# Performance work log

Hardware: AMD Instinct MI355X
Metric: run time of the kernel (lower is better)

## Reference

```python
import jax, jax.numpy as jnp
import numpy as np

B, S, H = 4, 2048, 1536
NH, HD = 12, 128          # num_heads, head_dim
K = 4                     # base_kernel
INNER = 4 * H             # GLU inner dim
EPS = 1e-6
CONV_DILS = (1, 2, 4, 8, 16, 32)
HEAD_DILS = [(1, 2, 4), (1, 1, 1), (4, 8, 16), (8, 16, 32), (32, 64, 128),
             (64, 128, 256), (256, 512, 1024), (1, 100, 200), (1, 500, 1000),
             (1, 1024, 2048), (3, 9, 27), (5, 25, 125)]


def setup_inputs() -> dict:
    key = jax.random.key(0)
    ks = jax.random.split(key, 20)
    sd = 0.02
    inp = {
        'x': jax.random.normal(ks[0], (B, S, H), dtype=jnp.float32),
        'norm_w': jnp.ones((3, H), dtype=jnp.float32),
        # DilatedConvStack: 6 depthwise convs (C=H, K=4) + proj Linear(H,H)
        'conv_ws': jax.random.normal(ks[1], (6, H, 1, K), dtype=jnp.float32) * sd,
        'conv_bs': jax.random.normal(ks[2], (6, H), dtype=jnp.float32) * sd,
        'conv_proj_w': jax.random.normal(ks[3], (H, H), dtype=jnp.float32) * sd,
        'conv_proj_b': jax.random.normal(ks[4], (H,), dtype=jnp.float32) * sd,
        # MultiHeadDilatedState
        'gate_w': jax.random.normal(ks[5], (2 * H, H), dtype=jnp.float32) * sd,
        'router_w': jax.random.normal(ks[6], (NH, H), dtype=jnp.float32) * sd,
        'router_b': jax.random.normal(ks[7], (NH,), dtype=jnp.float32) * sd,
        'head_ws': jax.random.normal(ks[8], (NH, 3, HD, 1, K), dtype=jnp.float32) * sd,
        'head_bs': jax.random.normal(ks[9], (NH, 3, HD), dtype=jnp.float32) * sd,
        'mix_gate_w': jax.random.normal(ks[10], (H, H), dtype=jnp.float32) * sd,
        'mix_gate_b': jnp.full((H,), 2.0, dtype=jnp.float32),
        'mixing_w': jax.random.normal(ks[11], (H, H), dtype=jnp.float32) * sd,
        'mixing_b': jax.random.normal(ks[12], (H,), dtype=jnp.float32) * sd,
        # GLU FFN
        'ffn_in_w': jax.random.normal(ks[13], (2 * INNER, H), dtype=jnp.float32) * sd,
        'ffn_out_w': jax.random.normal(ks[14], (H, INNER), dtype=jnp.float32) * sd,
        # path gates (Linear(H,1) x 3)
        'pg_w': jax.random.normal(ks[15], (3, H), dtype=jnp.float32) * sd,
        'pg_b': jnp.full((3,), 2.0, dtype=jnp.float32),
    }
    return inp


def rmsnorm(x, w):
    norm = jax.lax.rsqrt(jnp.mean(x * x, axis=-1, keepdims=True) + EPS)
    return x * norm * w


def dconv(h, w, b, d):
    # h: [B, C, S], w: [C, 1, K] depthwise, causal left-pad (K-1)*d
    C = h.shape[1]
    pad = (K - 1) * d
    y = jax.lax.conv_general_dilated(
        h, w, window_strides=(1,), padding=[(pad, 0)], rhs_dilation=(d,),
        dimension_numbers=('NCH', 'OIH', 'NCH'), feature_group_count=C)
    return y + b[None, :, None]


def reference(x, norm_w, conv_ws, conv_bs, conv_proj_w, conv_proj_b,
              gate_w, router_w, router_b, head_ws, head_bs,
              mix_gate_w, mix_gate_b, mixing_w, mixing_b,
              ffn_in_w, ffn_out_w, pg_w, pg_b):
    n1 = rmsnorm(x, norm_w[0])
    n2 = rmsnorm(x, norm_w[1])
    n3 = rmsnorm(x, norm_w[2])
    gc = jax.nn.sigmoid(jnp.einsum('bsh,h->bs', n1, pg_w[0]) + pg_b[0])[..., None]
    gs = jax.nn.sigmoid(jnp.einsum('bsh,h->bs', n2, pg_w[1]) + pg_b[1])[..., None]
    gf = jax.nn.sigmoid(jnp.einsum('bsh,h->bs', n3, pg_w[2]) + pg_b[2])[..., None]

    # --- DilatedConvStack path ---
    h = jnp.swapaxes(n1, 1, 2)  # [B, H, S]
    for i, d in enumerate(CONV_DILS):
        h = h + jax.nn.gelu(dconv(h, conv_ws[i], conv_bs[i], d), approximate=False)
    conv_out = jnp.swapaxes(h, 1, 2) @ conv_proj_w.T + conv_proj_b
    x = x + gc * conv_out

    # --- MultiHeadDilatedState path ---
    head_weights = jax.nn.sigmoid(n2 @ router_w.T + router_b)  # [B, S, NH]
    g = n2 @ gate_w.T                                          # [B, S, 2H]
    content, gate = jnp.split(g, 2, axis=-1)
    x_gated = content * jax.nn.sigmoid(gate)
    x_heads = x_gated.reshape(B, S, NH, HD)
    outs = []
    for i in range(NH):
        hh = jnp.swapaxes(x_heads[:, :, i, :], 1, 2)  # [B, HD, S]
        for j, d in enumerate(HEAD_DILS[i]):
            hh = hh + dconv(hh, head_ws[i, j], head_bs[i, j], d)
        hh = jnp.swapaxes(hh, 1, 2)                   # [B, S, HD]
        outs.append(hh * head_weights[:, :, i:i + 1])
    out = jnp.concatenate(outs, axis=-1)              # [B, S, H]
    out = out * jax.nn.sigmoid(out @ mix_gate_w.T + mix_gate_b)
    state_out = out @ mixing_w.T + mixing_b
    x = x + gs * state_out

    # --- GLU FFN path ---
    hff = n3 @ ffn_in_w.T
    c, gt = jnp.split(hff, 2, axis=-1)
    ffn_out = (c * jax.nn.sigmoid(gt)) @ ffn_out_w.T
    x = x + gf * ffn_out
    return x
```

## Files before the change

### kernel.cpp

```cpp
#include <hip/hip_runtime.h>
#include <stdint.h>

#define H 1536
#define SQ 2048
#define BB 4
#define MT 8192
#define NHD 12
#define INNER 6144
#define EPSF 1e-6f

typedef unsigned short u16;
typedef __bf16 b16x8 __attribute__((ext_vector_type(8)));
typedef float f32x4 __attribute__((ext_vector_type(4)));

__device__ __forceinline__ u16 f2b(float f) {
  uint32_t u = __float_as_uint(f);
  u = u + 0x7fffu + ((u >> 16) & 1u);
  return (u16)(u >> 16);
}
__device__ __forceinline__ float b2f(u16 u) { return __uint_as_float(((uint32_t)u) << 16); }
__device__ __forceinline__ float sigm(float x) { return 1.0f / (1.0f + __expf(-x)); }
__device__ __forceinline__ float gelu_exact(float x) {
  float z = fabsf(x) * 0.70710678118654752f;
  float t = 1.0f / (1.0f + 0.3275911f * z);
  float p = t * (0.254829592f + t * (-0.284496736f + t * (1.421413741f +
            t * (-1.453152027f + t * 1.061405429f))));
  float erfa = 1.0f - p * __expf(-z * z);
  float erfv = (x >= 0.f) ? erfa : -erfa;
  return 0.5f * x * (1.0f + erfv);
}
__device__ __forceinline__ void load_lds16(const void* g, void* l) {
  __builtin_amdgcn_global_load_lds(
      (__attribute__((address_space(1))) void*)(g),
      (__attribute__((address_space(3))) void*)(l), 16, 0, 0);
}

__global__ __launch_bounds__(256) void k_rmsnorm(const float* __restrict__ x, u16* __restrict__ xb) {
  int m = blockIdx.x, t = threadIdx.x;
  const float* row = x + (size_t)m * H;
  float v[6]; float ss = 0.f;
#pragma unroll
  for (int j = 0; j < 6; ++j) { v[j] = row[t + j * 256]; ss += v[j] * v[j]; }
#pragma unroll
  for (int o = 32; o > 0; o >>= 1) ss += __shfl_xor(ss, o);
  __shared__ float red[4];
  if ((t & 63) == 0) red[t >> 6] = ss;
  __syncthreads();
  float r = rsqrtf((red[0] + red[1] + red[2] + red[3]) / (float)H + EPSF);
#pragma unroll
  for (int j = 0; j < 6; ++j) xb[(size_t)m * H + t + j * 256] = f2b(v[j] * r);
}

__global__ __launch_bounds__(256) void k_gates(const u16* __restrict__ xb, const float* __restrict__ norm_w,
    const float* __restrict__ pg_w, const float* __restrict__ pg_b,
    const float* __restrict__ router_w, const float* __restrict__ router_b,
    float* __restrict__ gates, float* __restrict__ hw) {
  int m = blockIdx.x, t = threadIdx.x;
  const u16* row = xb + (size_t)m * H;
  float acc[15];
#pragma unroll
  for (int i = 0; i < 15; ++i) acc[i] = 0.f;
  for (int j = 0; j < 6; ++j) {
    int c = t + j * 256;
    float xv = b2f(row[c]);
    float n0 = norm_w[c], n1 = norm_w[H + c], n2 = norm_w[2 * H + c];
    acc[0] += xv * n0 * pg_w[c];
    acc[1] += xv * n1 * pg_w[H + c];
    acc[2] += xv * n2 * pg_w[2 * H + c];
    float xn = xv * n1;
#pragma unroll
    for (int i = 0; i < 12; ++i) acc[3 + i] += xn * router_w[(size_t)i * H + c];
  }
  __shared__ float red[15][4];
#pragma unroll
  for (int i = 0; i < 15; ++i) {
    float s = acc[i];
#pragma unroll
    for (int o = 32; o > 0; o >>= 1) s += __shfl_xor(s, o);
    if ((t & 63) == 0) red[i][t >> 6] = s;
  }
  __syncthreads();
  if (t < 15) {
    float s = red[t][0] + red[t][1] + red[t][2] + red[t][3];
    if (t < 3) gates[t * MT + m] = sigm(s + pg_b[t]);
    else hw[(size_t)m * NHD + (t - 3)] = sigm(s + router_b[t - 3]);
  }
}

__global__ __launch_bounds__(256) void k_wcvt(const float* __restrict__ w, u16* __restrict__ wb,
                                              const float* __restrict__ cs, int K) {
  int c = blockIdx.x * 256 + threadIdx.x;
  size_t r = blockIdx.y;
  float v = w[r * K + c];
  if (cs) v *= cs[c];
  wb[r * K + c] = f2b(v);
}
__global__ __launch_bounds__(256) void k_wcvt2(const float* __restrict__ w, u16* __restrict__ wb,
                                               const float* __restrict__ cs, int K, int HALF) {
  int c = blockIdx.x * 256 + threadIdx.x;
  int rr = blockIdx.y;
  int src = (rr & 1) ? (HALF + (rr >> 1)) : (rr >> 1);
  wb[(size_t)rr * K + c] = f2b(w[(size_t)src * K + c] * cs[c]);
}

__global__ __launch_bounds__(256) void k_conv(const u16* __restrict__ in, u16* __restrict__ out,
    const float* __restrict__ w, const float* __restrict__ bias, int d, const float* __restrict__ insc) {
  int c = blockIdx.x * 256 + threadIdx.x;
  int s0 = blockIdx.y * 8, b = blockIdx.z;
  float sc = insc ? insc[c] : 1.f;
  const u16* base = in + (size_t)b * SQ * H + c;
  u16* obase = out + (size_t)b * SQ * H + c;
  float4 wv = *(const float4*)(w + (size_t)c * 4);
  float bv = bias[c];
#pragma unroll
  for (int k = 0; k < 8; ++k) {
    int s = s0 + k;
    float center = b2f(base[(size_t)s * H]) * sc;
    float acc = bv + wv.w * center;
    if (s - d     >= 0) acc += wv.z * b2f(base[(size_t)(s - d) * H]) * sc;
    if (s - 2 * d >= 0) acc += wv.y * b2f(base[(size_t)(s - 2 * d) * H]) * sc;
    if (s - 3 * d >= 0) acc += wv.x * b2f(base[(size_t)(s - 3 * d) * H]) * sc;
    obase[(size_t)s * H] = f2b(center + gelu_exact(acc));
  }
}

__constant__ int HDILS[36] = {1,2,4, 1,1,1, 4,8,16, 8,16,32, 32,64,128, 64,128,256,
                              256,512,1024, 1,100,200, 1,500,1000, 1,1024,2048, 3,9,27, 5,25,125};

__global__ __launch_bounds__(256) void k_hconv(const u16* __restrict__ in, u16* __restrict__ out,
    const float* __restrict__ hws, const float* __restrict__ hbs, int j, const float* __restrict__ hwp) {
  int c = blockIdx.x * 256 + threadIdx.x;
  int s0 = blockIdx.y * 8, b = blockIdx.z;
  int head = c >> 7, cc = c & 127;
  int d = HDILS[head * 3 + j];
  size_t wi = (size_t)(head * 3 + j) * 128 + cc;
  float4 wv = *(const float4*)(hws + wi * 4);
  float bv = hbs[wi];
  const u16* base = in + (size_t)b * SQ * H + c;
  u16* obase = out + (size_t)b * SQ * H + c;
#pragma unroll
  for (int k = 0; k < 8; ++k) {
    int s = s0 + k;
    float center = b2f(base[(size_t)s * H]);
    float acc = bv + wv.w * center;
    if (s - d     >= 0) acc += wv.z * b2f(base[(size_t)(s - d) * H]);
    if (s - 2 * d >= 0) acc += wv.y * b2f(base[(size_t)(s - 2 * d) * H]);
    if (s - 3 * d >= 0) acc += wv.x * b2f(base[(size_t)(s - 3 * d) * H]);
    float v = center + acc;
    if (hwp) v *= hwp[((size_t)b * SQ + s) * NHD + head];
    obase[(size_t)s * H] = f2b(v);
  }
}

#define MMQ(AF, BF, MO, NO)                                                      \
  _Pragma("unroll") for (int m_ = 0; m_ < 4; ++m_)                               \
  _Pragma("unroll") for (int n_ = 0; n_ < 2; ++n_)                               \
  _Pragma("unroll") for (int ks_ = 0; ks_ < 2; ++ks_)                            \
    acc[(MO) + m_][(NO) + n_] = __builtin_amdgcn_mfma_f32_16x16x32_bf16(         \
        AF[m_][ks_], BF[n_][ks_], acc[(MO) + m_][(NO) + n_], 0, 0, 0);

#define TILE(BUF, SKO, DOSTAGE, VMSTMT)                                          \
  {                                                                              \
    b16x8 alo[4][2], ahi[4][2], blo[2][2], bhi[2][2];                            \
    _Pragma("unroll") for (int m = 0; m < 4; ++m) {                              \
      alo[m][0] = *(const b16x8*)(Ard0 + (BUF) * 16384 + m * 1024);              \
      alo[m][1] = *(const b16x8*)(Ard1 + (BUF) * 16384 + m * 1024);              \
    }                                                                            \
    _Pragma("unroll") for (int n = 0; n < 2; ++n) {                              \
      blo[n][0] = *(const b16x8*)(Brd0 + (BUF) * 16384 + n * 1024);              \
      blo[n][1] = *(const b16x8*)(Brd1 + (BUF) * 16384 + n * 1024);              \
    }                                                                            \
    asm volatile("s_waitcnt lgkmcnt(8)" ::: "memory");                           \
    __builtin_amdgcn_sched_barrier(0);                                           \
    __builtin_amdgcn_s_barrier();                                                \
    asm volatile("s_waitcnt lgkmcnt(0)" ::: "memory");                           \
    __builtin_amdgcn_sched_barrier(0);                                           \
    __builtin_amdgcn_s_setprio(1);                                               \
    MMQ(alo, blo, 0, 0);                                                         \
    __builtin_amdgcn_s_setprio(0);                                               \
    __builtin_amdgcn_sched_barrier(0);                                           \
    __builtin_amdgcn_s_barrier();                                                \
    _Pragma("unroll") for (int n = 0; n < 2; ++n) {                              \
      bhi[n][0] = *(const b16x8*)(Brd0 + (BUF) * 16384 + 2048 + n * 1024);       \
      bhi[n][1] = *(const b16x8*)(Brd1 + (BUF) * 16384 + 2048 + n * 1024);       \
    }                                                                            \
    __builtin_amdgcn_sched_barrier(0);                                           \
    __builtin_amdgcn_s_barrier();                                                \
    asm volatile("s_waitcnt lgkmcnt(0)" ::: "memory");                           \
    __builtin_amdgcn_sched_barrier(0);                                           \
    __builtin_amdgcn_s_setprio(1);                                               \
    MMQ(alo, bhi, 0, 2);                                                         \
    __builtin_amdgcn_s_setprio(0);                                               \
    __builtin_amdgcn_sched_barrier(0);                                           \
    __builtin_amdgcn_s_barrier();                                                \
    _Pragma("unroll") for (int m = 0; m < 4; ++m) {                              \
      ahi[m][0] = *(const b16x8*)(Ard0 + (BUF) * 16384 + 4096 + m * 1024);       \
      ahi[m][1] = *(const b16x8*)(Ard1 + (BUF) * 16384 + 4096 + m * 1024);       \
    }                                                                            \
    if (DOSTAGE) {                                                               \
      load_lds16(Bg + (boff0 + (SKO)), dB0 + (BUF) * 16384);                     \
      load_lds16(Bg + (boff1 + (SKO)), dB1 + (BUF) * 16384);                     \
      load_lds16(Bg + (boff2 + (SKO)), dB2 + (BUF) * 16384);                     \
      load_lds16(Bg + (boff3 + (SKO)), dB3 + (BUF) * 16384);                     \
    }                                                                            \
    __builtin_amdgcn_sched_barrier(0);                                           \
    __builtin_amdgcn_s_barrier();                                                \
    asm volatile("s_waitcnt lgkmcnt(0)" ::: "memory");                           \
    __builtin_amdgcn_sched_barrier(0);                                           \
    __builtin_amdgcn_s_setprio(1);                                               \
    MMQ(ahi, bhi, 4, 2);                                                         \
    __builtin_amdgcn_s_setprio(0);                                               \
    __builtin_amdgcn_sched_barrier(0);                                           \
    __builtin_amdgcn_s_barrier();                                                \
    if (DOSTAGE) {                                                               \
      load_lds16(Ag + (aoff0 + (SKO)), dA0 + (BUF) * 16384);                     \
      load_lds16(Ag + (aoff1 + (SKO)), dA1 + (BUF) * 16384);                     \
      load_lds16(Ag + (aoff2 + (SKO)), dA2 + (BUF) * 16384);                     \
      load_lds16(Ag + (aoff3 + (SKO)), dA3 + (BUF) * 16384);                     \
    }                                                                            \
    __builtin_amdgcn_sched_barrier(0);                                           \
    __builtin_amdgcn_s_barrier();                                                \
    __builtin_amdgcn_s_setprio(1);                                               \
    MMQ(ahi, blo, 4, 0);                                                         \
    __builtin_amdgcn_s_setprio(0);                                               \
    VMSTMT;                                                                      \
    __builtin_amdgcn_sched_barrier(0);                                           \
    __builtin_amdgcn_s_barrier();                                                \
  }

template<int MODE>
__global__ __launch_bounds__(512, 2) void k_gemm(const u16* __restrict__ A, int lda,
    const u16* __restrict__ B, int ldb, void* __restrict__ Cout, int M, int N, int K,
    const float* __restrict__ bias, const float* __restrict__ gate, const u16* __restrict__ aux,
    const float* __restrict__ xres) {
  __shared__ u16 lds[65536];
  int tid = threadIdx.x;
  int w = tid >> 6, lane = tid & 63;
  int l15 = lane & 15, l4 = lane >> 4;
  int wr = w >> 2, wc = w & 3;

  int gx = gridDim.x, gy = gridDim.y;
  int nwg = gx * gy;
  int bid = blockIdx.y * gx + blockIdx.x;
  int bm, bn;
  if (((nwg & 7) == 0) && ((gy & 7) == 0)) {
    int xcd = bid & 7, l = bid >> 3;
    int rpx = gy >> 3;
    bm = xcd * rpx + (l % rpx);
    bn = l / rpx;
  } else { bn = bid % gx; bm = bid / gx; }

  const u16* Ag = A + (size_t)bm * 256 * lda;
  const u16* Bg = B + (size_t)bn * 256 * ldb;
  int nt = K >> 6;

  f32x4 acc[8][4];
#pragma unroll
  for (int m = 0; m < 8; ++m)
#pragma unroll
    for (int n = 0; n < 4; ++n) acc[m][n] = f32x4{0.f, 0.f, 0.f, 0.f};

  int m7 = l15 & 7;
  int slot0 = l4 ^ m7, slot1 = slot0 ^ 4;
  const u16* Ard0 = lds + wr * 8192 + l15 * 64 + slot0 * 8;
  const u16* Ard1 = lds + wr * 8192 + l15 * 64 + slot1 * 8;
  const u16* Brd0 = lds + 32768 + (wc >> 1) * 8192 + ((wc & 1) * 64 + l15) * 64 + slot0 * 8;
  const u16* Brd1 = lds + 32768 + (wc >> 1) * 8192 + ((wc & 1) * 64 + l15) * 64 + slot1 * 8;

  int r0 = tid >> 3;
  int kg = ((lane & 7) ^ (lane >> 3)) * 8;
  int aoff0 = (0 * 128 + 0 * 64 + r0) * lda + kg;
  int aoff1 = (0 * 128 + 1 * 64 + r0) * lda + kg;
  int aoff2 = (1 * 128 + 0 * 64 + r0) * lda + kg;
  int aoff3 = (1 * 128 + 1 * 64 + r0) * lda + kg;
  int boff0 = (0 * 128 + 0 * 64 + r0) * ldb + kg;
  int boff1 = (0 * 128 + 1 * 64 + r0) * ldb + kg;
  int boff2 = (1 * 128 + 0 * 64 + r0) * ldb + kg;
  int boff3 = (1 * 128 + 1 * 64 + r0) * ldb + kg;
  int w512 = w * 512;
  u16* dA0 = lds + 0 * 4096 + w512;
  u16* dA1 = lds + 1 * 4096 + w512;
  u16* dA2 = lds + 2 * 4096 + w512;
  u16* dA3 = lds + 3 * 4096 + w512;
  u16* dB0 = lds + 32768 + 0 * 4096 + w512;
  u16* dB1 = lds + 32768 + 1 * 4096 + w512;
  u16* dB2 = lds + 32768 + 2 * 4096 + w512;
  u16* dB3 = lds + 32768 + 3 * 4096 + w512;

  load_lds16(Bg + boff0, dB0); load_lds16(Bg + boff1, dB1);
  load_lds16(Bg + boff2, dB2); load_lds16(Bg + boff3, dB3);
  load_lds16(Ag + aoff0, dA0); load_lds16(Ag + aoff1, dA1);
  load_lds16(Ag + aoff2, dA2); load_lds16(Ag + aoff3, dA3);
  load_lds16(Bg + boff0 + 64, dB0 + 16384); load_lds16(Bg + boff1 + 64, dB1 + 16384);
  load_lds16(Bg + boff2 + 64, dB2 + 16384); load_lds16(Bg + boff3 + 64, dB3 + 16384);
  load_lds16(Ag + aoff0 + 64, dA0 + 16384); load_lds16(Ag + aoff1 + 64, dA1 + 16384);
  load_lds16(Ag + aoff2 + 64, dA2 + 16384); load_lds16(Ag + aoff3 + 64, dA3 + 16384);
  asm volatile("s_waitcnt vmcnt(8)" ::: "memory");
  __builtin_amdgcn_s_barrier();
  __builtin_amdgcn_sched_barrier(0);

  int koff = 0;
  int main_iters = (nt >> 1) - 1;
  for (int it = 0; it < main_iters; ++it) {
    TILE(0, koff + 128, true, asm volatile("s_waitcnt vmcnt(8)" ::: "memory"));
    TILE(1, koff + 192, true, asm volatile("s_waitcnt vmcnt(8)" ::: "memory"));
    koff += 128;
  }
  TILE(0, 0, false, asm volatile("s_waitcnt vmcnt(0)" ::: "memory"));
  TILE(1, 0, false, (void)0);

  int rowbase = bm * 256 + wr * 128;
  int colbase = bn * 256 + wc * 64;
#pragma unroll
  for (int n = 0; n < 4; ++n) {
    int col = colbase + n * 16 + l15;
    float bv = (MODE == 2) ? 0.f : (bias ? bias[col] : 0.f);
#pragma unroll
    for (int m = 0; m < 8; ++m) {
#pragma unroll
      for (int j = 0; j < 4; ++j) {
        int r = rowbase + m * 16 + l4 * 4 + j;
        float val = acc[m][n][j];
        if (MODE == 0) {
          size_t idx = (size_t)r * N + col;
          ((float*)Cout)[idx] = xres[idx] + (val + bv) * gate[r];
        } else if (MODE == 1) {
          ((float*)Cout)[(size_t)r * N + col] += (val + bv) * (gate ? gate[r] : 1.f);
        } else if (MODE == 2) {
          float other = __shfl_xor(val, 1);
          if ((lane & 1) == 0)
            ((u16*)Cout)[(size_t)r * (N >> 1) + (col >> 1)] = f2b(val * sigm(other));
        } else {
          float a = b2f(aux[(size_t)r * N + col]);
          ((u16*)Cout)[(size_t)r * N + col] = f2b(a * sigm(val + bv));
        }
      }
    }
  }
}

extern "C" void kernel_launch(void* const* d_in, const int* in_sizes, int n_in,
                              void* d_out, int out_size, void* d_ws, size_t ws_size,
                              hipStream_t stream) {
  const float* x        = (const float*)d_in[0];
  const float* norm_w   = (const float*)d_in[1];
  const float* conv_ws  = (const float*)d_in[2];
  const float* conv_bs  = (const float*)d_in[3];
  const float* conv_pw  = (const float*)d_in[4];
  const float* conv_pb  = (const float*)d_in[5];
  const float* gate_w   = (const float*)d_in[6];
  const float* router_w = (const float*)d_in[7];
  const float* router_b = (const float*)d_in[8];
  const float* head_ws  = (const float*)d_in[9];
  const float* head_bs  = (const float*)d_in[10];
  const float* mixg_w   = (const float*)d_in[11];
  const float* mixg_b   = (const float*)d_in[12];
  const float* mix_w    = (const float*)d_in[13];
  const float* mix_b    = (const float*)d_in[14];
  const float* ffn_iw   = (const float*)d_in[15];
  const float* ffn_ow   = (const float*)d_in[16];
  const float* pg_w     = (const float*)d_in[17];
  const float* pg_b     = (const float*)d_in[18];
  float* out = (float*)d_out;

  char* ws = (char*)d_ws;
  size_t o = 0;
  auto alloc = [&](size_t n) { char* p = ws + o; o += n; return p; };
  u16*  XB  = (u16*)alloc(25165824);
  u16*  A16 = (u16*)alloc(25165824);
  u16*  B16 = (u16*)alloc(25165824);
  u16*  WG2 = (u16*)alloc(9437184);
  u16*  WP  = (u16*)alloc(4718592);
  u16*  WMG = (u16*)alloc(4718592);
  u16*  WMX = (u16*)alloc(4718592);
  u16*  WFI = (u16*)alloc(37748736);
  u16*  WFO = (u16*)alloc(18874368);
  float* gates = (float*)alloc(98304);
  float* hw    = (float*)alloc(393216);
  u16*  VB = A16;

  k_rmsnorm<<<MT, 256, 0, stream>>>(x, XB);
  k_gates<<<MT, 256, 0, stream>>>(XB, norm_w, pg_w, pg_b, router_w, router_b, gates, hw);

  k_wcvt2<<<dim3(6, 3072),  256, 0, stream>>>(gate_w, WG2, norm_w + H, H, H);
  k_wcvt <<<dim3(6, 1536),  256, 0, stream>>>(conv_pw, WP, nullptr, H);
  k_wcvt <<<dim3(6, 1536),  256, 0, stream>>>(mixg_w, WMG, nullptr, H);
  k_wcvt <<<dim3(6, 1536),  256, 0, stream>>>(mix_w, WMX, nullptr, H);
  k_wcvt2<<<dim3(6, 12288), 256, 0, stream>>>(ffn_iw, WFI, norm_w + 2 * H, H, INNER);
  k_wcvt <<<dim3(24, 1536), 256, 0, stream>>>(ffn_ow, WFO, nullptr, INNER);

  dim3 cg(6, SQ / 8, BB);
  k_conv<<<cg, 256, 0, stream>>>(XB,  A16, conv_ws + 0 * H * 4, conv_bs + 0 * H, 1,  norm_w);
  k_conv<<<cg, 256, 0, stream>>>(A16, B16, conv_ws + 1 * H * 4, conv_bs + 1 * H, 2,  nullptr);
  k_conv<<<cg, 256, 0, stream>>>(B16, A16, conv_ws + 2 * H * 4, conv_bs + 2 * H, 4,  nullptr);
  k_conv<<<cg, 256, 0, stream>>>(A16, B16, conv_ws + 3 * H * 4, conv_bs + 3 * H, 8,  nullptr);
  k_conv<<<cg, 256, 0, stream>>>(B16, A16, conv_ws + 4 * H * 4, conv_bs + 4 * H, 16, nullptr);
  k_conv<<<cg, 256, 0, stream>>>(A16, B16, conv_ws + 5 * H * 4, conv_bs + 5 * H, 32, nullptr);
  k_gemm<0><<<dim3(6, 32), 512, 0, stream>>>(B16, H, WP, H, out, MT, H, H, conv_pb, gates, nullptr, x);

  k_gemm<2><<<dim3(12, 32), 512, 0, stream>>>(XB, H, WG2, H, A16, MT, 2 * H, H, nullptr, nullptr, nullptr, nullptr);
  k_hconv<<<cg, 256, 0, stream>>>(A16, B16, head_ws, head_bs, 0, nullptr);
  k_hconv<<<cg, 256, 0, stream>>>(B16, A16, head_ws, head_bs, 1, nullptr);
  k_hconv<<<cg, 256, 0, stream>>>(A16, B16, head_ws, head_bs, 2, hw);
  k_gemm<3><<<dim3(6, 32), 512, 0, stream>>>(B16, H, WMG, H, A16, MT, H, H, mixg_b, nullptr, B16, nullptr);
  k_gemm<1><<<dim3(6, 32), 512, 0, stream>>>(A16, H, WMX, H, out, MT, H, H, mix_b, gates + MT, nullptr, nullptr);

  for (int ch = 0; ch < 2; ++ch) {
    k_gemm<2><<<dim3(24, 32), 512, 0, stream>>>(XB, H, WFI + (size_t)ch * 6144 * H, H,
                                                VB, MT, 6144, H, nullptr, nullptr, nullptr, nullptr);
    k_gemm<1><<<dim3(6, 32), 512, 0, stream>>>(VB, 3072, WFO + ch * 3072, INNER,
                                               out, MT, H, 3072, nullptr, gates + 2 * MT, nullptr, nullptr);
  }
}
```

Baseline: 1.317 ms.

## Fuse pairs of dilated conv layers and batch gate rows per block

Pairs of consecutive dilated depthwise convolutions (the six conv-stack layers and the first two head-conv layers) now run in one kernel each. Every output recomputes the four first-layer taps it needs, which removes an intermediate bf16 round trip through global memory and some launches. The cost is about four times the first-layer loads and GELU evaluations per output, now done by one thread per sequence position. The gates kernel handles 16 rows per block and precomputes the norm-weight products once per block. The three HxH weight conversions are merged into a single launch.

```diff
diff --git a/kernel.cpp b/kernel.cpp
--- a/kernel.cpp
+++ b/kernel.cpp
@@ -51,39 +51,50 @@
   for (int j = 0; j < 6; ++j) xb[(size_t)m * H + t + j * 256] = f2b(v[j] * r);
 }
 
-__global__ __launch_bounds__(256) void k_gates(const u16* __restrict__ xb, const float* __restrict__ norm_w,
+__global__ __launch_bounds__(256) void k_gates16(const u16* __restrict__ xb, const float* __restrict__ norm_w,
     const float* __restrict__ pg_w, const float* __restrict__ pg_b,
     const float* __restrict__ router_w, const float* __restrict__ router_b,
     float* __restrict__ gates, float* __restrict__ hw) {
-  int m = blockIdx.x, t = threadIdx.x;
-  const u16* row = xb + (size_t)m * H;
-  float acc[15];
-#pragma unroll
-  for (int i = 0; i < 15; ++i) acc[i] = 0.f;
+  int t = threadIdx.x;
+  int m0 = blockIdx.x * 16;
+  float pm[6][15];
+#pragma unroll
   for (int j = 0; j < 6; ++j) {
     int c = t + j * 256;
-    float xv = b2f(row[c]);
     float n0 = norm_w[c], n1 = norm_w[H + c], n2 = norm_w[2 * H + c];
-    acc[0] += xv * n0 * pg_w[c];
-    acc[1] += xv * n1 * pg_w[H + c];
-    acc[2] += xv * n2 * pg_w[2 * H + c];
-    float xn = xv * n1;
-#pragma unroll
-    for (int i = 0; i < 12; ++i) acc[3 + i] += xn * router_w[(size_t)i * H + c];
+    pm[j][0] = n0 * pg_w[c];
+    pm[j][1] = n1 * pg_w[H + c];
+    pm[j][2] = n2 * pg_w[2 * H + c];
+#pragma unroll
+    for (int i = 0; i < 12; ++i) pm[j][3 + i] = n1 * router_w[(size_t)i * H + c];
   }
   __shared__ float red[15][4];
-#pragma unroll
-  for (int i = 0; i < 15; ++i) {
-    float s = acc[i];
-#pragma unroll
-    for (int o = 32; o > 0; o >>= 1) s += __shfl_xor(s, o);
-    if ((t & 63) == 0) red[i][t >> 6] = s;
-  }
-  __syncthreads();
-  if (t < 15) {
-    float s = red[t][0] + red[t][1] + red[t][2] + red[t][3];
-    if (t < 3) gates[t * MT + m] = sigm(s + pg_b[t]);
-    else hw[(size_t)m * NHD + (t - 3)] = sigm(s + router_b[t - 3]);
+  for (int tk = 0; tk < 16; ++tk) {
+    int m = m0 + tk;
+    const u16* row = xb + (size_t)m * H;
+    float acc[15];
+#pragma unroll
+    for (int i = 0; i < 15; ++i) acc[i] = 0.f;
+#pragma unroll
+    for (int j = 0; j < 6; ++j) {
+      float xv = b2f(row[t + j * 256]);
+#pragma unroll
+      for (int i = 0; i < 15; ++i) acc[i] += xv * pm[j][i];
+    }
+#pragma unroll
+    for (int i = 0; i < 15; ++i) {
+      float s = acc[i];
+#pragma unroll
+      for (int o = 32; o > 0; o >>= 1) s += __shfl_xor(s, o);
+      if ((t & 63) == 0) red[i][t >> 6] = s;
+    }
+    __syncthreads();
+    if (t < 15) {
+      float s = red[t][0] + red[t][1] + red[t][2] + red[t][3];
+      if (t < 3) gates[t * MT + m] = sigm(s + pg_b[t]);
+      else hw[(size_t)m * NHD + (t - 3)] = sigm(s + router_b[t - 3]);
+    }
+    __syncthreads();
   }
 }
 
@@ -102,30 +113,74 @@
   int src = (rr & 1) ? (HALF + (rr >> 1)) : (rr >> 1);
   wb[(size_t)rr * K + c] = f2b(w[(size_t)src * K + c] * cs[c]);
 }
-
-__global__ __launch_bounds__(256) void k_conv(const u16* __restrict__ in, u16* __restrict__ out,
-    const float* __restrict__ w, const float* __restrict__ bias, int d, const float* __restrict__ insc) {
-  int c = blockIdx.x * 256 + threadIdx.x;
-  int s0 = blockIdx.y * 8, b = blockIdx.z;
+__global__ __launch_bounds__(256) void k_wcvt3(const float* __restrict__ w0, const float* __restrict__ w1,
+                                               const float* __restrict__ w2, u16* __restrict__ wb) {
+  int c = blockIdx.x * 256 + threadIdx.x;
+  int r = blockIdx.y;
+  const float* src = (r < 1536) ? w0 : (r < 3072 ? w1 : w2);
+  int rr = (r < 1536) ? r : (r < 3072 ? r - 1536 : r - 3072);
+  wb[(size_t)r * H + c] = f2b(src[(size_t)rr * H + c]);
+}
+
+__global__ __launch_bounds__(256) void k_conv2(const u16* __restrict__ in, u16* __restrict__ out,
+    const float* __restrict__ w0p, const float* __restrict__ b0p,
+    const float* __restrict__ w1p, const float* __restrict__ b1p,
+    int d0, int d1, const float* __restrict__ insc) {
+  int c = blockIdx.x * 256 + threadIdx.x;
+  int s = blockIdx.y, b = blockIdx.z;
   float sc = insc ? insc[c] : 1.f;
   const u16* base = in + (size_t)b * SQ * H + c;
-  u16* obase = out + (size_t)b * SQ * H + c;
-  float4 wv = *(const float4*)(w + (size_t)c * 4);
-  float bv = bias[c];
-#pragma unroll
-  for (int k = 0; k < 8; ++k) {
-    int s = s0 + k;
-    float center = b2f(base[(size_t)s * H]) * sc;
-    float acc = bv + wv.w * center;
-    if (s - d     >= 0) acc += wv.z * b2f(base[(size_t)(s - d) * H]) * sc;
-    if (s - 2 * d >= 0) acc += wv.y * b2f(base[(size_t)(s - 2 * d) * H]) * sc;
-    if (s - 3 * d >= 0) acc += wv.x * b2f(base[(size_t)(s - 3 * d) * H]) * sc;
-    obase[(size_t)s * H] = f2b(center + gelu_exact(acc));
-  }
+  float4 wv0 = *(const float4*)(w0p + (size_t)c * 4);
+  float4 wv1 = *(const float4*)(w1p + (size_t)c * 4);
+  float b0 = b0p[c], b1 = b1p[c];
+  float h1v[4];
+#pragma unroll
+  for (int k = 0; k < 4; ++k) {
+    int r = s - k * d1;
+    if (r >= 0) {
+      float center = b2f(base[(size_t)r * H]) * sc;
+      float a = b0 + wv0.w * center;
+      if (r - d0     >= 0) a += wv0.z * b2f(base[(size_t)(r - d0) * H]) * sc;
+      if (r - 2 * d0 >= 0) a += wv0.y * b2f(base[(size_t)(r - 2 * d0) * H]) * sc;
+      if (r - 3 * d0 >= 0) a += wv0.x * b2f(base[(size_t)(r - 3 * d0) * H]) * sc;
+      h1v[k] = center + gelu_exact(a);
+    } else h1v[k] = 0.f;
+  }
+  float a1 = b1 + wv1.w * h1v[0] + wv1.z * h1v[1] + wv1.y * h1v[2] + wv1.x * h1v[3];
+  out[((size_t)b * SQ + s) * H + c] = f2b(h1v[0] + gelu_exact(a1));
 }
 
 __constant__ int HDILS[36] = {1,2,4, 1,1,1, 4,8,16, 8,16,32, 32,64,128, 64,128,256,
                               256,512,1024, 1,100,200, 1,500,1000, 1,1024,2048, 3,9,27, 5,25,125};
+
+__global__ __launch_bounds__(256) void k_hconv2(const u16* __restrict__ in, u16* __restrict__ out,
+    const float* __restrict__ hws, const float* __restrict__ hbs) {
+  int c = blockIdx.x * 256 + threadIdx.x;
+  int s = blockIdx.y, b = blockIdx.z;
+  int head = c >> 7, cc = c & 127;
+  int d0 = HDILS[head * 3 + 0], d1 = HDILS[head * 3 + 1];
+  size_t wi0 = (size_t)(head * 3 + 0) * 128 + cc;
+  size_t wi1 = (size_t)(head * 3 + 1) * 128 + cc;
+  float4 wv0 = *(const float4*)(hws + wi0 * 4);
+  float4 wv1 = *(const float4*)(hws + wi1 * 4);
+  float b0 = hbs[wi0], b1 = hbs[wi1];
+  const u16* base = in + (size_t)b * SQ * H + c;
+  float h1v[4];
+#pragma unroll
+  for (int k = 0; k < 4; ++k) {
+    int r = s - k * d1;
+    if (r >= 0) {
+      float center = b2f(base[(size_t)r * H]);
+      float a = b0 + wv0.w * center;
+      if (r - d0     >= 0) a += wv0.z * b2f(base[(size_t)(r - d0) * H]);
+      if (r - 2 * d0 >= 0) a += wv0.y * b2f(base[(size_t)(r - 2 * d0) * H]);
+      if (r - 3 * d0 >= 0) a += wv0.x * b2f(base[(size_t)(r - 3 * d0) * H]);
+      h1v[k] = center + a;
+    } else h1v[k] = 0.f;
+  }
+  float a1 = b1 + wv1.w * h1v[0] + wv1.z * h1v[1] + wv1.y * h1v[2] + wv1.x * h1v[3];
+  out[((size_t)b * SQ + s) * H + c] = f2b(h1v[0] + a1);
+}
 
 __global__ __launch_bounds__(256) void k_hconv(const u16* __restrict__ in, u16* __restrict__ out,
     const float* __restrict__ hws, const float* __restrict__ hbs, int j, const float* __restrict__ hwp) {
@@ -380,28 +435,25 @@
   u16*  VB = A16;
 
   k_rmsnorm<<<MT, 256, 0, stream>>>(x, XB);
-  k_gates<<<MT, 256, 0, stream>>>(XB, norm_w, pg_w, pg_b, router_w, router_b, gates, hw);
+  k_gates16<<<MT / 16, 256, 0, stream>>>(XB, norm_w, pg_w, pg_b, router_w, router_b, gates, hw);
 
   k_wcvt2<<<dim3(6, 3072),  256, 0, stream>>>(gate_w, WG2, norm_w + H, H, H);
-  k_wcvt <<<dim3(6, 1536),  256, 0, stream>>>(conv_pw, WP, nullptr, H);
-  k_wcvt <<<dim3(6, 1536),  256, 0, stream>>>(mixg_w, WMG, nullptr, H);
-  k_wcvt <<<dim3(6, 1536),  256, 0, stream>>>(mix_w, WMX, nullptr, H);
+  k_wcvt3<<<dim3(6, 4608),  256, 0, stream>>>(conv_pw, mixg_w, mix_w, WP);
   k_wcvt2<<<dim3(6, 12288), 256, 0, stream>>>(ffn_iw, WFI, norm_w + 2 * H, H, INNER);
   k_wcvt <<<dim3(24, 1536), 256, 0, stream>>>(ffn_ow, WFO, nullptr, INNER);
 
-  dim3 cg(6, SQ / 8, BB);
-  k_conv<<<cg, 256, 0, stream>>>(XB,  A16, conv_ws + 0 * H * 4, conv_bs + 0 * H, 1,  norm_w);
-  k_conv<<<cg, 256, 0, stream>>>(A16, B16, conv_ws + 1 * H * 4, conv_bs + 1 * H, 2,  nullptr);
-  k_conv<<<cg, 256, 0, stream>>>(B16, A16, conv_ws + 2 * H * 4, conv_bs + 2 * H, 4,  nullptr);
-  k_conv<<<cg, 256, 0, stream>>>(A16, B16, conv_ws + 3 * H * 4, conv_bs + 3 * H, 8,  nullptr);
-  k_conv<<<cg, 256, 0, stream>>>(B16, A16, conv_ws + 4 * H * 4, conv_bs + 4 * H, 16, nullptr);
-  k_conv<<<cg, 256, 0, stream>>>(A16, B16, conv_ws + 5 * H * 4, conv_bs + 5 * H, 32, nullptr);
-  k_gemm<0><<<dim3(6, 32), 512, 0, stream>>>(B16, H, WP, H, out, MT, H, H, conv_pb, gates, nullptr, x);
-
-  k_gemm<2><<<dim3(12, 32), 512, 0, stream>>>(XB, H, WG2, H, A16, MT, 2 * H, H, nullptr, nullptr, nullptr, nullptr);
-  k_hconv<<<cg, 256, 0, stream>>>(A16, B16, head_ws, head_bs, 0, nullptr);
-  k_hconv<<<cg, 256, 0, stream>>>(B16, A16, head_ws, head_bs, 1, nullptr);
-  k_hconv<<<cg, 256, 0, stream>>>(A16, B16, head_ws, head_bs, 2, hw);
+  dim3 cg1(6, SQ, BB);
+  k_conv2<<<cg1, 256, 0, stream>>>(XB,  A16, conv_ws + 0 * H * 4, conv_bs + 0 * H,
+                                   conv_ws + 1 * H * 4, conv_bs + 1 * H, 1, 2, norm_w);
+  k_conv2<<<cg1, 256, 0, stream>>>(A16, B16, conv_ws + 2 * H * 4, conv_bs + 2 * H,
+                                   conv_ws + 3 * H * 4, conv_bs + 3 * H, 4, 8, nullptr);
+  k_conv2<<<cg1, 256, 0, stream>>>(B16, A16, conv_ws + 4 * H * 4, conv_bs + 4 * H,
+                                   conv_ws + 5 * H * 4, conv_bs + 5 * H, 16, 32, nullptr);
+  k_gemm<0><<<dim3(6, 32), 512, 0, stream>>>(A16, H, WP, H, out, MT, H, H, conv_pb, gates, nullptr, x);
+
+  k_gemm<2><<<dim3(12, 32), 512, 0, stream>>>(XB, H, WG2, H, B16, MT, 2 * H, H, nullptr, nullptr, nullptr, nullptr);
+  k_hconv2<<<cg1, 256, 0, stream>>>(B16, A16, head_ws, head_bs);
+  k_hconv<<<dim3(6, SQ / 8, BB), 256, 0, stream>>>(A16, B16, head_ws, head_bs, 2, hw);
   k_gemm<3><<<dim3(6, 32), 512, 0, stream>>>(B16, H, WMG, H, A16, MT, H, H, mixg_b, nullptr, B16, nullptr);
   k_gemm<1><<<dim3(6, 32), 512, 0, stream>>>(A16, H, WMX, H, out, MT, H, H, mix_b, gates + MT, nullptr, nullptr);
 
```

Result: slower. 1.464 ms (+11.2%).

## Batch gate rows per block, merge weight casts, unchunk FFN when workspace allows

Applied to the files above, without the earlier changes.

The gates kernel now handles 16 rows per block and precomputes the norm-weighted projection coefficients once per block rather than once per row. The three square weight conversions are merged into a single launch. When the workspace can hold the full GLU intermediate, the FFN runs as one up-projection GEMM and one down-projection GEMM instead of two chunks of each, which cuts launches and read-modify-write passes over the output. The cost is an extra 96MB workspace buffer and a K=6144 down-projection GEMM whose single accumulation pass may behave differently.

```diff
diff --git a/kernel.cpp b/kernel.cpp
--- a/kernel.cpp
+++ b/kernel.cpp
@@ -51,39 +51,50 @@
   for (int j = 0; j < 6; ++j) xb[(size_t)m * H + t + j * 256] = f2b(v[j] * r);
 }
 
-__global__ __launch_bounds__(256) void k_gates(const u16* __restrict__ xb, const float* __restrict__ norm_w,
+__global__ __launch_bounds__(256) void k_gates16(const u16* __restrict__ xb, const float* __restrict__ norm_w,
     const float* __restrict__ pg_w, const float* __restrict__ pg_b,
     const float* __restrict__ router_w, const float* __restrict__ router_b,
     float* __restrict__ gates, float* __restrict__ hw) {
-  int m = blockIdx.x, t = threadIdx.x;
-  const u16* row = xb + (size_t)m * H;
-  float acc[15];
-#pragma unroll
-  for (int i = 0; i < 15; ++i) acc[i] = 0.f;
+  int t = threadIdx.x;
+  int m0 = blockIdx.x * 16;
+  float pm[6][15];
+#pragma unroll
   for (int j = 0; j < 6; ++j) {
     int c = t + j * 256;
-    float xv = b2f(row[c]);
     float n0 = norm_w[c], n1 = norm_w[H + c], n2 = norm_w[2 * H + c];
-    acc[0] += xv * n0 * pg_w[c];
-    acc[1] += xv * n1 * pg_w[H + c];
-    acc[2] += xv * n2 * pg_w[2 * H + c];
-    float xn = xv * n1;
-#pragma unroll
-    for (int i = 0; i < 12; ++i) acc[3 + i] += xn * router_w[(size_t)i * H + c];
+    pm[j][0] = n0 * pg_w[c];
+    pm[j][1] = n1 * pg_w[H + c];
+    pm[j][2] = n2 * pg_w[2 * H + c];
+#pragma unroll
+    for (int i = 0; i < 12; ++i) pm[j][3 + i] = n1 * router_w[(size_t)i * H + c];
   }
   __shared__ float red[15][4];
-#pragma unroll
-  for (int i = 0; i < 15; ++i) {
-    float s = acc[i];
-#pragma unroll
-    for (int o = 32; o > 0; o >>= 1) s += __shfl_xor(s, o);
-    if ((t & 63) == 0) red[i][t >> 6] = s;
-  }
-  __syncthreads();
-  if (t < 15) {
-    float s = red[t][0] + red[t][1] + red[t][2] + red[t][3];
-    if (t < 3) gates[t * MT + m] = sigm(s + pg_b[t]);
-    else hw[(size_t)m * NHD + (t - 3)] = sigm(s + router_b[t - 3]);
+  for (int tk = 0; tk < 16; ++tk) {
+    int m = m0 + tk;
+    const u16* row = xb + (size_t)m * H;
+    float acc[15];
+#pragma unroll
+    for (int i = 0; i < 15; ++i) acc[i] = 0.f;
+#pragma unroll
+    for (int j = 0; j < 6; ++j) {
+      float xv = b2f(row[t + j * 256]);
+#pragma unroll
+      for (int i = 0; i < 15; ++i) acc[i] += xv * pm[j][i];
+    }
+#pragma unroll
+    for (int i = 0; i < 15; ++i) {
+      float s = acc[i];
+#pragma unroll
+      for (int o = 32; o > 0; o >>= 1) s += __shfl_xor(s, o);
+      if ((t & 63) == 0) red[i][t >> 6] = s;
+    }
+    __syncthreads();
+    if (t < 15) {
+      float s = red[t][0] + red[t][1] + red[t][2] + red[t][3];
+      if (t < 3) gates[t * MT + m] = sigm(s + pg_b[t]);
+      else hw[(size_t)m * NHD + (t - 3)] = sigm(s + router_b[t - 3]);
+    }
+    __syncthreads();
   }
 }
 
@@ -101,6 +112,14 @@
   int rr = blockIdx.y;
   int src = (rr & 1) ? (HALF + (rr >> 1)) : (rr >> 1);
   wb[(size_t)rr * K + c] = f2b(w[(size_t)src * K + c] * cs[c]);
+}
+__global__ __launch_bounds__(256) void k_wcvt3(const float* __restrict__ w0, const float* __restrict__ w1,
+                                               const float* __restrict__ w2, u16* __restrict__ wb) {
+  int c = blockIdx.x * 256 + threadIdx.x;
+  int r = blockIdx.y;
+  const float* src = (r < 1536) ? w0 : (r < 3072 ? w1 : w2);
+  int rr = (r < 1536) ? r : (r < 3072 ? r - 1536 : r - 3072);
+  wb[(size_t)r * H + c] = f2b(src[(size_t)rr * H + c]);
 }
 
 __global__ __launch_bounds__(256) void k_conv(const u16* __restrict__ in, u16* __restrict__ out,
@@ -378,14 +397,15 @@
   float* gates = (float*)alloc(98304);
   float* hw    = (float*)alloc(393216);
   u16*  VB = A16;
+  size_t base_end = o;
+  bool bigws = (ws_size >= base_end + 100663296ull);
+  u16* VBX = bigws ? (u16*)alloc(100663296) : nullptr;
 
   k_rmsnorm<<<MT, 256, 0, stream>>>(x, XB);
-  k_gates<<<MT, 256, 0, stream>>>(XB, norm_w, pg_w, pg_b, router_w, router_b, gates, hw);
+  k_gates16<<<MT / 16, 256, 0, stream>>>(XB, norm_w, pg_w, pg_b, router_w, router_b, gates, hw);
 
   k_wcvt2<<<dim3(6, 3072),  256, 0, stream>>>(gate_w, WG2, norm_w + H, H, H);
-  k_wcvt <<<dim3(6, 1536),  256, 0, stream>>>(conv_pw, WP, nullptr, H);
-  k_wcvt <<<dim3(6, 1536),  256, 0, stream>>>(mixg_w, WMG, nullptr, H);
-  k_wcvt <<<dim3(6, 1536),  256, 0, stream>>>(mix_w, WMX, nullptr, H);
+  k_wcvt3<<<dim3(6, 4608),  256, 0, stream>>>(conv_pw, mixg_w, mix_w, WP);
   k_wcvt2<<<dim3(6, 12288), 256, 0, stream>>>(ffn_iw, WFI, norm_w + 2 * H, H, INNER);
   k_wcvt <<<dim3(24, 1536), 256, 0, stream>>>(ffn_ow, WFO, nullptr, INNER);
 
@@ -405,10 +425,17 @@
   k_gemm<3><<<dim3(6, 32), 512, 0, stream>>>(B16, H, WMG, H, A16, MT, H, H, mixg_b, nullptr, B16, nullptr);
   k_gemm<1><<<dim3(6, 32), 512, 0, stream>>>(A16, H, WMX, H, out, MT, H, H, mix_b, gates + MT, nullptr, nullptr);
 
-  for (int ch = 0; ch < 2; ++ch) {
-    k_gemm<2><<<dim3(24, 32), 512, 0, stream>>>(XB, H, WFI + (size_t)ch * 6144 * H, H,
-                                                VB, MT, 6144, H, nullptr, nullptr, nullptr, nullptr);
-    k_gemm<1><<<dim3(6, 32), 512, 0, stream>>>(VB, 3072, WFO + ch * 3072, INNER,
-                                               out, MT, H, 3072, nullptr, gates + 2 * MT, nullptr, nullptr);
-  }
-}
+  if (bigws) {
+    k_gemm<2><<<dim3(48, 32), 512, 0, stream>>>(XB, H, WFI, H, VBX, MT, 2 * INNER, H,
+                                                nullptr, nullptr, nullptr, nullptr);
+    k_gemm<1><<<dim3(6, 32), 512, 0, stream>>>(VBX, INNER, WFO, INNER, out, MT, H, INNER,
+                                               nullptr, gates + 2 * MT, nullptr, nullptr);
+  } else {
+    for (int ch = 0; ch < 2; ++ch) {
+      k_gemm<2><<<dim3(24, 32), 512, 0, stream>>>(XB, H, WFI + (size_t)ch * 6144 * H, H,
+                                                  VB, MT, 6144, H, nullptr, nullptr, nullptr, nullptr);
+      k_gemm<1><<<dim3(6, 32), 512, 0, stream>>>(VB, 3072, WFO + ch * 3072, INNER,
+                                                 out, MT, H, 3072, nullptr, gates + 2 * MT, nullptr, nullptr);
+    }
+  }
+}
```

Measured after the change: 1.380 ms. 1.05x slower.

## Merge conv-proj, state-gate and full FFN-in GEMMs into one grouped launch

Applied to the files above, without the earlier changes.

Moves the GEMM body into a device function and adds a grouped kernel. One launch now runs the conv projection, the state gate GEMM and the whole FFN input GEMM as separate tile ranges. With enough workspace, the full FFN intermediate goes to a new 96 MiB buffer and the FFN output becomes a single K=6144 GEMM instead of two chunked passes. The aim is to cut launch count and tail underuse by packing independent GEMMs into one grid. The cost is extra workspace traffic and a fallback path when the workspace is small.

```diff
diff --git a/kernel.cpp b/kernel.cpp
--- a/kernel.cpp
+++ b/kernel.cpp
@@ -229,26 +229,14 @@
   }
 
 template<int MODE>
-__global__ __launch_bounds__(512, 2) void k_gemm(const u16* __restrict__ A, int lda,
-    const u16* __restrict__ B, int ldb, void* __restrict__ Cout, int M, int N, int K,
+__device__ __forceinline__ void gemm_body(u16* lds, const u16* __restrict__ A, int lda,
+    const u16* __restrict__ B, int ldb, void* __restrict__ Cout, int N, int K,
     const float* __restrict__ bias, const float* __restrict__ gate, const u16* __restrict__ aux,
-    const float* __restrict__ xres) {
-  __shared__ u16 lds[65536];
+    const float* __restrict__ xres, int bm, int bn) {
   int tid = threadIdx.x;
   int w = tid >> 6, lane = tid & 63;
   int l15 = lane & 15, l4 = lane >> 4;
   int wr = w >> 2, wc = w & 3;
-
-  int gx = gridDim.x, gy = gridDim.y;
-  int nwg = gx * gy;
-  int bid = blockIdx.y * gx + blockIdx.x;
-  int bm, bn;
-  if (((nwg & 7) == 0) && ((gy & 7) == 0)) {
-    int xcd = bid & 7, l = bid >> 3;
-    int rpx = gy >> 3;
-    bm = xcd * rpx + (l % rpx);
-    bn = l / rpx;
-  } else { bn = bid % gx; bm = bid / gx; }
 
   const u16* Ag = A + (size_t)bm * 256 * lda;
   const u16* Bg = B + (size_t)bn * 256 * ldb;
@@ -336,6 +324,49 @@
         }
       }
     }
+  }
+}
+
+__device__ __forceinline__ void swz_seg(int l, int gx, int gy, int& bm, int& bn) {
+  int xcd = l & 7, q = l >> 3;
+  int rpx = gy >> 3;
+  bm = xcd * rpx + (q % rpx);
+  bn = q / rpx;
+}
+
+template<int MODE>
+__global__ __launch_bounds__(512, 2) void k_gemm(const u16* __restrict__ A, int lda,
+    const u16* __restrict__ B, int ldb, void* __restrict__ Cout, int M, int N, int K,
+    const float* __restrict__ bias, const float* __restrict__ gate, const u16* __restrict__ aux,
+    const float* __restrict__ xres) {
+  __shared__ u16 lds[65536];
+  int gx = gridDim.x, gy = gridDim.y;
+  int nwg = gx * gy;
+  int bid = blockIdx.y * gx + blockIdx.x;
+  int bm, bn;
+  if (((nwg & 7) == 0) && ((gy & 7) == 0)) {
+    swz_seg(bid, gx, gy, bm, bn);
+  } else { bn = bid % gx; bm = bid / gx; }
+  gemm_body<MODE>(lds, A, lda, B, ldb, Cout, N, K, bias, gate, aux, xres, bm, bn);
+}
+
+__global__ __launch_bounds__(512, 2) void k_gemm3(
+    const u16* __restrict__ Acp, const u16* __restrict__ Wcp, float* __restrict__ Cout_,
+    const float* __restrict__ cp_bias, const float* __restrict__ cp_gate, const float* __restrict__ xres,
+    const u16* __restrict__ XB, const u16* __restrict__ WG2, u16* __restrict__ Cgate,
+    const u16* __restrict__ WFI, u16* __restrict__ Cffn) {
+  __shared__ u16 lds[65536];
+  int bid = blockIdx.x;
+  int bm, bn;
+  if (bid < 192) {
+    swz_seg(bid, 6, 32, bm, bn);
+    gemm_body<0>(lds, Acp, H, Wcp, H, Cout_, 1536, 1536, cp_bias, cp_gate, nullptr, xres, bm, bn);
+  } else if (bid < 576) {
+    swz_seg(bid - 192, 12, 32, bm, bn);
+    gemm_body<2>(lds, XB, H, WG2, H, Cgate, 3072, 1536, nullptr, nullptr, nullptr, nullptr, bm, bn);
+  } else {
+    swz_seg(bid - 576, 48, 32, bm, bn);
+    gemm_body<2>(lds, XB, H, WFI, H, Cffn, 12288, 1536, nullptr, nullptr, nullptr, nullptr, bm, bn);
   }
 }
 
@@ -378,6 +409,9 @@
   float* gates = (float*)alloc(98304);
   float* hw    = (float*)alloc(393216);
   u16*  VB = A16;
+  size_t base_end = o;
+  bool bigws = (ws_size >= base_end + 100663296ull);
+  u16* VX = bigws ? (u16*)alloc(100663296) : nullptr;
 
   k_rmsnorm<<<MT, 256, 0, stream>>>(x, XB);
   k_gates<<<MT, 256, 0, stream>>>(XB, norm_w, pg_w, pg_b, router_w, router_b, gates, hw);
@@ -396,19 +430,30 @@
   k_conv<<<cg, 256, 0, stream>>>(A16, B16, conv_ws + 3 * H * 4, conv_bs + 3 * H, 8,  nullptr);
   k_conv<<<cg, 256, 0, stream>>>(B16, A16, conv_ws + 4 * H * 4, conv_bs + 4 * H, 16, nullptr);
   k_conv<<<cg, 256, 0, stream>>>(A16, B16, conv_ws + 5 * H * 4, conv_bs + 5 * H, 32, nullptr);
-  k_gemm<0><<<dim3(6, 32), 512, 0, stream>>>(B16, H, WP, H, out, MT, H, H, conv_pb, gates, nullptr, x);
-
-  k_gemm<2><<<dim3(12, 32), 512, 0, stream>>>(XB, H, WG2, H, A16, MT, 2 * H, H, nullptr, nullptr, nullptr, nullptr);
+
+  if (bigws) {
+    k_gemm3<<<2112, 512, 0, stream>>>(B16, WP, out, conv_pb, gates, x,
+                                      XB, WG2, A16, WFI, VX);
+  } else {
+    k_gemm<0><<<dim3(6, 32), 512, 0, stream>>>(B16, H, WP, H, out, MT, H, H, conv_pb, gates, nullptr, x);
+    k_gemm<2><<<dim3(12, 32), 512, 0, stream>>>(XB, H, WG2, H, A16, MT, 2 * H, H, nullptr, nullptr, nullptr, nullptr);
+  }
+
   k_hconv<<<cg, 256, 0, stream>>>(A16, B16, head_ws, head_bs, 0, nullptr);
   k_hconv<<<cg, 256, 0, stream>>>(B16, A16, head_ws, head_bs, 1, nullptr);
   k_hconv<<<cg, 256, 0, stream>>>(A16, B16, head_ws, head_bs, 2, hw);
   k_gemm<3><<<dim3(6, 32), 512, 0, stream>>>(B16, H, WMG, H, A16, MT, H, H, mixg_b, nullptr, B16, nullptr);
   k_gemm<1><<<dim3(6, 32), 512, 0, stream>>>(A16, H, WMX, H, out, MT, H, H, mix_b, gates + MT, nullptr, nullptr);
 
-  for (int ch = 0; ch < 2; ++ch) {
-    k_gemm<2><<<dim3(24, 32), 512, 0, stream>>>(XB, H, WFI + (size_t)ch * 6144 * H, H,
-                                                VB, MT, 6144, H, nullptr, nullptr, nullptr, nullptr);
-    k_gemm<1><<<dim3(6, 32), 512, 0, stream>>>(VB, 3072, WFO + ch * 3072, INNER,
-                                               out, MT, H, 3072, nullptr, gates + 2 * MT, nullptr, nullptr);
-  }
-}
+  if (bigws) {
+    k_gemm<1><<<dim3(6, 32), 512, 0, stream>>>(VX, INNER, WFO, INNER, out, MT, H, INNER,
+                                               nullptr, gates + 2 * MT, nullptr, nullptr);
+  } else {
+    for (int ch = 0; ch < 2; ++ch) {
+      k_gemm<2><<<dim3(24, 32), 512, 0, stream>>>(XB, H, WFI + (size_t)ch * 6144 * H, H,
+                                                  VB, MT, 6144, H, nullptr, nullptr, nullptr, nullptr);
+      k_gemm<1><<<dim3(6, 32), 512, 0, stream>>>(VB, 3072, WFO + ch * 3072, INNER,
+                                                 out, MT, H, 3072, nullptr, gates + 2 * MT, nullptr, nullptr);
+    }
+  }
+}
```

Result: slower. 1.354 ms (+2.8%).
